# Kernel tuning notes

Measured on AMD Instinct MI355X. Metric: run time of the kernel, lower is better.

The kernel has to match this reference:

```python
import jax, jax.numpy as jnp
import numpy as np

B, S, D, H = 2, 1024, 1024, 16
HD = D // H
WINDOW = 256
FFN = 4 * D


def setup_inputs() -> dict:
    key = jax.random.key(0)
    ks = jax.random.split(key, 12)
    xav = lambda k, o, i: jax.random.normal(k, (o, i), jnp.float32) * np.sqrt(2.0 / (o + i))
    return {
        "x": jax.random.normal(ks[0], (B, S, D), jnp.float32),
        "wq": xav(ks[1], D, D), "bq": jnp.zeros((D,), jnp.float32),
        "wk": xav(ks[2], D, D), "bk": jnp.zeros((D,), jnp.float32),
        "wv": xav(ks[3], D, D), "bv": jnp.zeros((D,), jnp.float32),
        "wo": xav(ks[4], D, D), "bo": jnp.zeros((D,), jnp.float32),
        "attn_norm_w": jnp.ones((D,), jnp.float32),
        "ffn_norm_w": jnp.ones((D,), jnp.float32),
        "gate_w": xav(ks[5], FFN, D),
        "up_w": xav(ks[6], FFN, D),
        "down_w": xav(ks[7], D, FFN),
    }


def _rms(x, w):
    return x * jax.lax.rsqrt(jnp.mean(x * x, axis=-1, keepdims=True) + 1e-6) * w


def _rotate_half(x):
    x1, x2 = jnp.split(x, 2, axis=-1)
    return jnp.concatenate([-x2, x1], axis=-1)


def _rope_cos_sin(seq_len, head_dim):
    inv_freq = 1.0 / (10000.0 ** (jnp.arange(0, head_dim, 2, dtype=jnp.float32) / head_dim))
    freqs = jnp.arange(seq_len, dtype=jnp.float32)[:, None] * inv_freq[None, :]  # [S, HD/2]
    emb = jnp.concatenate([freqs, freqs], axis=-1)  # [S, HD]
    return jnp.cos(emb)[None, None], jnp.sin(emb)[None, None]  # [1,1,S,HD]


def reference(x, wq, bq, wk, bk, wv, bv, wo, bo, attn_norm_w, ffn_norm_w, gate_w, up_w, down_w):
    b, s, d = x.shape
    scale = 1.0 / np.sqrt(HD)
    residual = x
    h = _rms(x, attn_norm_w)
    q = (h @ wq.T + bq).reshape(b, s, H, HD).transpose(0, 2, 1, 3)  # [B,H,S,HD]
    k = (h @ wk.T + bk).reshape(b, s, H, HD).transpose(0, 2, 1, 3)
    v = (h @ wv.T + bv).reshape(b, s, H, HD).transpose(0, 2, 1, 3)
    cos, sin = _rope_cos_sin(s, HD)
    q = q * cos + _rotate_half(q) * sin
    k = k * cos + _rotate_half(k) * sin
    scores = jnp.einsum("bhqd,bhkd->bhqk", q, k) * scale  # dense [B,H,S,S]
    i = jnp.arange(s)[:, None]
    j = jnp.arange(s)[None, :]
    local_mask = (j <= i) & (i - j < WINDOW)  # causal sliding window
    scores = jnp.where(local_mask[None, None], scores, -jnp.inf)
    attn = jax.nn.softmax(scores, axis=-1)
    out = jnp.einsum("bhqk,bhkd->bhqd", attn, v)
    out = out.transpose(0, 2, 1, 3).reshape(b, s, d) @ wo.T + bo
    x = residual + out
    residual = x
    h = _rms(x, ffn_norm_w)
    ffn = (jax.nn.silu(h @ gate_w.T) * (h @ up_w.T)) @ down_w.T
    return (residual + ffn, attn)
```

## Files before the change

kernel.cpp:

```cpp
#include <hip/hip_runtime.h>

typedef unsigned short u16;
typedef unsigned int u32;
typedef __attribute__((ext_vector_type(8))) short short8;
typedef __attribute__((ext_vector_type(4))) float f32x4;

__device__ __forceinline__ float b2fu(u32 u) {
  union { u32 i; float f; } v; v.i = u << 16; return v.f;
}
__device__ __forceinline__ u16 f2bu(float f) {
  union { float f; u32 i; } v; v.f = f;
  u32 r = (v.i + 0x7fffu + ((v.i >> 16) & 1u)) >> 16;
  return (u16)r;
}
__device__ __forceinline__ void gl_lds16(const void* g, void* l) {
  __builtin_amdgcn_global_load_lds((const __attribute__((address_space(1))) void*)g,
                                   (__attribute__((address_space(3))) void*)l, 16, 0, 0);
}
__device__ __forceinline__ short8 ld_lds_b8(const u16* p) {
  uint2 a = *(const uint2*)p;
  uint2 b = *(const uint2*)(p + 4);
  union { u32 u[4]; short8 s; } v;
  v.u[0] = a.x; v.u[1] = a.y; v.u[2] = b.x; v.u[3] = b.y;
  return v.s;
}

__global__ __launch_bounds__(256) void cvt_weights(
    const float* __restrict__ wq, const float* __restrict__ wk,
    const float* __restrict__ wv, const float* __restrict__ wo,
    const float* __restrict__ wg, const float* __restrict__ wu,
    const float* __restrict__ wd, u16* __restrict__ dst,
    const float* __restrict__ bq, const float* __restrict__ bk,
    const float* __restrict__ bv, float* __restrict__ bqkv)
{
  if (blockIdx.x >= 16384) {
    const int s = blockIdx.x - 16384;
    const float* bsrc = (s == 0) ? bq : (s == 1) ? bk : bv;
    const int o = threadIdx.x * 4;
    *(float4*)(bqkv + s * 1024 + o) = *(const float4*)(bsrc + o);
    return;
  }
  size_t e = ((size_t)blockIdx.x * 256 + threadIdx.x) * 4;
  size_t seg = e >> 20;
  const float* src; size_t soff;
  if      (seg == 0) { src = wq; soff = e; }
  else if (seg == 1) { src = wk; soff = e - ((size_t)1 << 20); }
  else if (seg == 2) { src = wv; soff = e - ((size_t)2 << 20); }
  else if (seg == 3) { src = wo; soff = e - ((size_t)3 << 20); }
  else if (seg < 12) {
    size_t idx = e - ((size_t)4 << 20);
    int rc = (int)(idx >> 10);
    int col = (int)(idx & 1023);
    int bi = rc >> 5, j = rc & 31;
    if (j < 16) { src = wg; soff = (size_t)(bi * 16 + j) * 1024 + col; }
    else        { src = wu; soff = (size_t)(bi * 16 + j - 16) * 1024 + col; }
  }
  else { src = wd; soff = e - ((size_t)12 << 20); }
  float4 v = *(const float4*)(src + soff);
  *(ushort4*)(dst + e) = make_ushort4(f2bu(v.x), f2bu(v.y), f2bu(v.z), f2bu(v.w));
}

__global__ __launch_bounds__(256) void rmsnorm_kernel(
    const float* __restrict__ x, const float* __restrict__ w, u16* __restrict__ out)
{
  const int row = blockIdx.x;
  const int t = threadIdx.x;
  float4 v = ((const float4*)(x + (size_t)row * 1024))[t];
  float ss = v.x * v.x + v.y * v.y + v.z * v.z + v.w * v.w;
#pragma unroll
  for (int m = 32; m > 0; m >>= 1) ss += __shfl_xor(ss, m, 64);
  __shared__ float red[4];
  if ((t & 63) == 0) red[t >> 6] = ss;
  __syncthreads();
  float tot = red[0] + red[1] + red[2] + red[3];
  float r = rsqrtf(tot * (1.0f / 1024.0f) + 1e-6f);
  float4 wv = ((const float4*)w)[t];
  ushort4 o = make_ushort4(f2bu(v.x * r * wv.x), f2bu(v.y * r * wv.y),
                           f2bu(v.z * r * wv.z), f2bu(v.w * r * wv.w));
  ((ushort4*)(out + (size_t)row * 1024))[t] = o;
}

template<int TMB, int TNB, int EPI, bool HAS_BIAS, bool HAS_RES, bool SPLIT>
__global__ __launch_bounds__(256) void gemm_bt(
    const u16* __restrict__ A, const u16* __restrict__ B, float* __restrict__ C,
    const float* __restrict__ bias, const float* __restrict__ res,
    int M, int N, int K, int lda,
    u16* __restrict__ P0, u16* __restrict__ P1, u16* __restrict__ P2)
{
  constexpr int BK = 32;
  constexpr int WTM = TMB / 2, WTN = TNB / 2;
  constexpr int MT = WTM / 16, NT = WTN / 16;
  __shared__ u16 As[TMB * BK];
  __shared__ u16 Bs[TNB * BK];
  const int t = threadIdx.x;
  const int w = t >> 6, l = t & 63;
  const int wm = (w >> 1) * WTM, wn = (w & 1) * WTN;
  const int lr = l & 15, lq = l >> 4;
  const int tile_m = blockIdx.y * TMB, tile_n = blockIdx.x * TNB;
  const int kb = SPLIT ? blockIdx.z * K : 0;
  if (SPLIT) C += (size_t)blockIdx.z * M * N;

  f32x4 acc[MT][NT] = {};

  const int sr = t >> 2;
  const int scs = (((t & 3) ^ ((t >> 3) & 3)) * 8);
  const int rsw = (lq ^ ((lr >> 1) & 3)) * 8;
  const u16* Ab = A + (size_t)(tile_m + sr) * lda + kb + scs;
  const u16* Bb = B + (size_t)(tile_n + sr) * lda + kb + scs;

  for (int kk = 0; kk < K; kk += BK) {
#pragma unroll
    for (int i = 0; i < TMB / 64; ++i)
      gl_lds16(Ab + kk + (size_t)i * 64 * lda, &As[t * 8 + i * 2048]);
#pragma unroll
    for (int i = 0; i < TNB / 64; ++i)
      gl_lds16(Bb + kk + (size_t)i * 64 * lda, &Bs[t * 8 + i * 2048]);
    __syncthreads();
    short8 af[MT], bfr[NT];
#pragma unroll
    for (int mt = 0; mt < MT; ++mt)
      af[mt] = *(const short8*)&As[(wm + mt * 16 + lr) * BK + rsw];
#pragma unroll
    for (int nt = 0; nt < NT; ++nt)
      bfr[nt] = *(const short8*)&Bs[(wn + nt * 16 + lr) * BK + rsw];
#pragma unroll
    for (int mt = 0; mt < MT; ++mt)
#pragma unroll
      for (int nt = 0; nt < NT; ++nt)
        acc[mt][nt] = __builtin_amdgcn_mfma_f32_16x16x32_bf16(af[mt], bfr[nt], acc[mt][nt], 0, 0, 0);
    __syncthreads();
  }

  if (EPI == 0) {
#pragma unroll
    for (int nt = 0; nt < NT; ++nt) {
      const int col = tile_n + wn + nt * 16 + lr;
      const float bv = HAS_BIAS ? bias[col] : 0.0f;
#pragma unroll
      for (int mt = 0; mt < MT; ++mt) {
        const int row0 = tile_m + wm + mt * 16 + lq * 4;
#pragma unroll
        for (int r = 0; r < 4; ++r) {
          const size_t off = (size_t)(row0 + r) * N + col;
          float v = acc[mt][nt][r] + bv;
          if (HAS_RES) v += res[off];
          C[off] = v;
        }
      }
    }
  } else if (EPI == 1) {
    const int colbase = tile_n + wn;
    const int seg = colbase >> 10;
    const int h = (colbase >> 6) & 15;
    u16* dstb = (seg == 0) ? P0 : (seg == 1) ? P1 : P2;
    float bv[NT];
#pragma unroll
    for (int nt = 0; nt < NT; ++nt) bv[nt] = bias[colbase + nt * 16 + lr];
#pragma unroll
    for (int mt = 0; mt < MT; ++mt) {
      const int row0 = tile_m + wm + mt * 16 + lq * 4;
#pragma unroll
      for (int r = 0; r < 4; ++r) {
        const int row = row0 + r;
        const int s = row & 1023, b = row >> 10;
        u16* dst = dstb + (((size_t)(b * 16 + h) << 10) + s) * 64;
        if (seg < 2) {
#pragma unroll
          for (int np = 0; np < 2; ++np) {
            const int i = np * 16 + lr;
            const float th = (float)s * exp2f(-0.4152410118609203f * (float)i);
            float sn, cs; __sincosf(th, &sn, &cs);
            const float g0 = acc[mt][np][r] + bv[np];
            const float g2 = acc[mt][np + 2][r] + bv[np + 2];
            dst[i]      = f2bu(g0 * cs - g2 * sn);
            dst[i + 32] = f2bu(g2 * cs + g0 * sn);
          }
        } else {
#pragma unroll
          for (int nt = 0; nt < NT; ++nt)
            dst[nt * 16 + lr] = f2bu(acc[mt][nt][r] + bv[nt]);
        }
      }
    }
  } else {
#pragma unroll
    for (int nt = 0; nt < NT; nt += 2) {
      const int feat = (((tile_n + wn + nt * 16) >> 5) << 4) + lr;
#pragma unroll
      for (int mt = 0; mt < MT; ++mt) {
        const int row0 = tile_m + wm + mt * 16 + lq * 4;
#pragma unroll
        for (int r = 0; r < 4; ++r) {
          const float g = acc[mt][nt][r];
          const float u = acc[mt][nt + 1][r];
          const float a = g / (1.0f + __expf(-g)) * u;
          P0[(size_t)(row0 + r) * (N >> 1) + feat] = f2bu(a);
        }
      }
    }
  }
}

#define FPH(buf, kk, mth, dostage, dovm) do {                                                  \
    if ((mth) == 0) {                                                                          \
      _Pragma("unroll")                                                                        \
      for (int nt = 0; nt < 4; ++nt)                                                           \
        bfr[nt] = *(const short8*)&Bs[(buf) * 16384 + (wn + nt * 16 + lr) * 64 +               \
                                      (((kk) * 32 + lq * 8) ^ cxor)];                          \
    }                                                                                          \
    short8 af[4];                                                                              \
    _Pragma("unroll")                                                                          \
    for (int mt = 0; mt < 4; ++mt)                                                             \
      af[mt] = *(const short8*)&As[(buf) * 16384 + (wm + (mth) * 64 + mt * 16 + lr) * 64 +     \
                                   (((kk) * 32 + lq * 8) ^ cxor)];                             \
    if (dostage) STAGE_ALL(kt + 1);                                                            \
    __builtin_amdgcn_s_barrier();                                                              \
    asm volatile("s_waitcnt lgkmcnt(0)" ::: "memory");                                         \
    __builtin_amdgcn_sched_barrier(0);                                                         \
    __builtin_amdgcn_s_setprio(1);                                                             \
    _Pragma("unroll")                                                                          \
    for (int mt = 0; mt < 4; ++mt)                                                             \
      _Pragma("unroll")                                                                        \
      for (int nt = 0; nt < 4; ++nt)                                                           \
        acc[(mth) * 4 + mt][nt] =                                                              \
            __builtin_amdgcn_mfma_f32_16x16x32_bf16(af[mt], bfr[nt], acc[(mth) * 4 + mt][nt],  \
                                                    0, 0, 0);                                  \
    __builtin_amdgcn_s_setprio(0);                                                             \
    if (dovm) asm volatile("s_waitcnt vmcnt(0)" ::: "memory");                                 \
    __builtin_amdgcn_s_barrier();                                                              \
  } while (0)

__global__ __launch_bounds__(512, 2) void ffn1_8ph(
    const u16* __restrict__ A, const u16* __restrict__ B, u16* __restrict__ act)
{
  __shared__ u16 As[32768];
  __shared__ u16 Bs[32768];
  const int t = threadIdx.x;
  const int wid = t >> 6, l = t & 63;
  const int lr = l & 15, lq = l >> 4;
  const int wm = (wid >> 2) * 128, wn = (wid & 3) * 64;
  const int tile_m = blockIdx.y * 256, tile_n = blockIdx.x * 256;
  const int cxor = (lr & 7) * 8;

  const int srow = t >> 3;
  const int schunk = (t & 7) ^ (srow & 7);
  const u16* aRow = A + (size_t)(tile_m + srow) * 1024 + schunk * 8;
  const u16* bRow = B + (size_t)(tile_n + srow) * 1024 + schunk * 8;

  auto STAGE_ALL = [&](int kt2) {
    if (kt2 < 16) {
      const int bz2 = kt2 & 1;
      const u16* ga = aRow + kt2 * 64;
      const u16* gb = bRow + kt2 * 64;
      u16* da = As + bz2 * 16384 + t * 8;
      u16* db = Bs + bz2 * 16384 + t * 8;
      gl_lds16(ga, da);
      gl_lds16(ga + 64 * 1024, da + 4096);
      gl_lds16(ga + 128 * 1024, da + 8192);
      gl_lds16(ga + 192 * 1024, da + 12288);
      gl_lds16(gb, db);
      gl_lds16(gb + 64 * 1024, db + 4096);
      gl_lds16(gb + 128 * 1024, db + 8192);
      gl_lds16(gb + 192 * 1024, db + 12288);
    }
  };

  f32x4 acc[8][4] = {};
  short8 bfr[4];

  STAGE_ALL(0);
  asm volatile("s_waitcnt vmcnt(0)" ::: "memory");
  __builtin_amdgcn_s_barrier();

  for (int kt = 0; kt < 16; ++kt) {
    const int bz = kt & 1;
    FPH(bz, 0, 0, 1, 0);
    FPH(bz, 0, 1, 0, 0);
    FPH(bz, 1, 0, 0, 0);
    FPH(bz, 1, 1, 0, 1);
  }

#pragma unroll
  for (int nt = 0; nt < 4; nt += 2) {
    const int feat = (((tile_n + wn + nt * 16) >> 5) << 4) + lr;
#pragma unroll
    for (int mi = 0; mi < 8; ++mi) {
      const int row0 = tile_m + wm + mi * 16 + lq * 4;
#pragma unroll
      for (int r = 0; r < 4; ++r) {
        const float g = acc[mi][nt][r];
        const float u = acc[mi][nt + 1][r];
        const float a = g / (1.0f + __expf(-g)) * u;
        act[(size_t)(row0 + r) * 4096 + feat] = f2bu(a);
      }
    }
  }
}

__global__ __launch_bounds__(256) void reduce4_kernel(
    const float* __restrict__ p, const float* __restrict__ res, float* __restrict__ out)
{
  const size_t i = ((size_t)blockIdx.x * 256 + threadIdx.x) * 4;
  float4 a = *(const float4*)(p + i);
  float4 b = *(const float4*)(p + i + 2097152);
  float4 c = *(const float4*)(p + i + 2 * 2097152);
  float4 d = *(const float4*)(p + i + 3 * 2097152);
  float4 r = *(const float4*)(res + i);
  float4 o;
  o.x = r.x + a.x + b.x + c.x + d.x;
  o.y = r.y + a.y + b.y + c.y + d.y;
  o.z = r.z + a.z + b.z + c.z + d.z;
  o.w = r.w + a.w + b.w + c.w + d.w;
  *(float4*)(out + i) = o;
}

#define KP 68
#define PP 296

__global__ __launch_bounds__(256) void attn_kernel(
    const u16* __restrict__ qb, const u16* __restrict__ kb, const u16* __restrict__ vb,
    float* __restrict__ probs, u16* __restrict__ ctx)
{
  __shared__ u16 Kbuf[288 * KP];
  __shared__ u16 Vbuf[288 * KP];
  __shared__ float smax[2][32];
  __shared__ float ssum[2][32];
  u16* Pbuf = Kbuf;

  const int blk = blockIdx.x;
  const int qt = blk & 31, bh = blk >> 5;
  const int b = bh >> 4, h = bh & 15;
  const int q0 = qt << 5;
  const int kstart = (q0 >= 256) ? (q0 - 256) : 0;
  const int kend = q0 + 32;
  const int span = kend - kstart;
  const int t = threadIdx.x;
  const int w = t >> 6, l = t & 63;
  const int lr = l & 15, lq = l >> 4;
  const int mw = w & 1, nh = w >> 1;
  const size_t bhS = (size_t)bh << 10;

  {
    const u16* kg = kb + ((bhS + (size_t)kstart) << 6);
    const u16* vg = vb + ((bhS + (size_t)kstart) << 6);
    for (int idx = t; idx < 288 * 8; idx += 256) {
      const int r = idx >> 3, c = (idx & 7) << 3;
      uint4 kv4 = make_uint4(0, 0, 0, 0), vv4 = make_uint4(0, 0, 0, 0);
      if (r < span) {
        kv4 = *(const uint4*)&kg[(r << 6) + c];
        vv4 = *(const uint4*)&vg[(r << 6) + c];
      }
      *(uint2*)&Kbuf[r * KP + c]     = make_uint2(kv4.x, kv4.y);
      *(uint2*)&Kbuf[r * KP + c + 4] = make_uint2(kv4.z, kv4.w);
      *(uint2*)&Vbuf[r * KP + c]     = make_uint2(vv4.x, vv4.y);
      *(uint2*)&Vbuf[r * KP + c + 4] = make_uint2(vv4.z, vv4.w);
    }
  }
  short8 qa0, qa1;
  {
    const u16* qrow = qb + ((bhS + (size_t)(q0 + mw * 16 + lr)) << 6) + lq * 8;
    qa0 = *(const short8*)qrow;
    qa1 = *(const short8*)(qrow + 32);
  }
  __syncthreads();

  f32x4 acc[9];
#pragma unroll
  for (int i = 0; i < 9; ++i) acc[i] = (f32x4){0.f, 0.f, 0.f, 0.f};
#pragma unroll
  for (int i = 0; i < 9; ++i) {
    const int nt = nh + 2 * i;
    const u16* kr = &Kbuf[(nt * 16 + lr) * KP + lq * 8];
    short8 kf0 = ld_lds_b8(kr);
    short8 kf1 = ld_lds_b8(kr + 32);
    acc[i] = __builtin_amdgcn_mfma_f32_16x16x32_bf16(qa0, kf0, acc[i], 0, 0, 0);
    acc[i] = __builtin_amdgcn_mfma_f32_16x16x32_bf16(qa1, kf1, acc[i], 0, 0, 0);
  }

  const int rbase = mw * 16 + lq * 4;
  float rmax[4] = {-1e30f, -1e30f, -1e30f, -1e30f};
#pragma unroll
  for (int i = 0; i < 9; ++i) {
    const int jg = kstart + (nh + 2 * i) * 16 + lr;
#pragma unroll
    for (int r = 0; r < 4; ++r) {
      const int q = q0 + rbase + r;
      const bool valid = (jg >= q - 255) && (jg <= q);
      const float v = valid ? acc[i][r] * 0.125f : -1e30f;
      acc[i][r] = v;
      rmax[r] = fmaxf(rmax[r], v);
    }
  }
#pragma unroll
  for (int r = 0; r < 4; ++r) {
    float m_ = rmax[r];
    m_ = fmaxf(m_, __shfl_xor(m_, 1, 64));
    m_ = fmaxf(m_, __shfl_xor(m_, 2, 64));
    m_ = fmaxf(m_, __shfl_xor(m_, 4, 64));
    m_ = fmaxf(m_, __shfl_xor(m_, 8, 64));
    rmax[r] = m_;
  }
  if (lr == 0) {
#pragma unroll
    for (int r = 0; r < 4; ++r) smax[nh][rbase + r] = rmax[r];
  }
  __syncthreads();
#pragma unroll
  for (int r = 0; r < 4; ++r)
    rmax[r] = fmaxf(smax[0][rbase + r], smax[1][rbase + r]);
  float rsum[4] = {0.f, 0.f, 0.f, 0.f};
#pragma unroll
  for (int i = 0; i < 9; ++i)
#pragma unroll
    for (int r = 0; r < 4; ++r) {
      const float p = exp2f((acc[i][r] - rmax[r]) * 1.44269504f);
      acc[i][r] = p;
      rsum[r] += p;
    }
#pragma unroll
  for (int r = 0; r < 4; ++r) {
    float s_ = rsum[r];
    s_ += __shfl_xor(s_, 1, 64);
    s_ += __shfl_xor(s_, 2, 64);
    s_ += __shfl_xor(s_, 4, 64);
    s_ += __shfl_xor(s_, 8, 64);
    rsum[r] = s_;
  }
  if (lr == 0) {
#pragma unroll
    for (int r = 0; r < 4; ++r) ssum[nh][rbase + r] = rsum[r];
  }
  __syncthreads();

  float inv4[4];
#pragma unroll
  for (int r = 0; r < 4; ++r)
    inv4[r] = 1.0f / (ssum[0][rbase + r] + ssum[1][rbase + r]);
#pragma unroll
  for (int i = 0; i < 9; ++i) {
    const int nt = nh + 2 * i;
#pragma unroll
    for (int r = 0; r < 4; ++r)
      Pbuf[(rbase + r) * PP + nt * 16 + lr] = f2bu(acc[i][r] * inv4[r]);
  }
  __syncthreads();

  {
    const int row = t >> 3;
    const int q = q0 + row;
    const int lo = q - 255;
    const int j8 = (t & 7) << 3;
    const u16* pr0 = &Pbuf[row * PP];
    float* prow = probs + ((bhS + (size_t)q) << 10);
#pragma unroll
    for (int k = 0; k < 16; ++k) {
      const int c = j8 + (k << 6);
      float4 o0 = make_float4(0.f, 0.f, 0.f, 0.f);
      float4 o1 = make_float4(0.f, 0.f, 0.f, 0.f);
      if (c >= kstart && c < kend) {
        union { uint4 v; u16 s[8]; } pv;
        pv.v = *(const uint4*)&pr0[c - kstart];
        o0.x = (c + 0 >= lo && c + 0 <= q) ? b2fu(pv.s[0]) : 0.0f;
        o0.y = (c + 1 >= lo && c + 1 <= q) ? b2fu(pv.s[1]) : 0.0f;
        o0.z = (c + 2 >= lo && c + 2 <= q) ? b2fu(pv.s[2]) : 0.0f;
        o0.w = (c + 3 >= lo && c + 3 <= q) ? b2fu(pv.s[3]) : 0.0f;
        o1.x = (c + 4 >= lo && c + 4 <= q) ? b2fu(pv.s[4]) : 0.0f;
        o1.y = (c + 5 >= lo && c + 5 <= q) ? b2fu(pv.s[5]) : 0.0f;
        o1.z = (c + 6 >= lo && c + 6 <= q) ? b2fu(pv.s[6]) : 0.0f;
        o1.w = (c + 7 >= lo && c + 7 <= q) ? b2fu(pv.s[7]) : 0.0f;
      }
      *(float4*)&prow[c] = o0;
      *(float4*)&prow[c + 4] = o1;
    }
  }

  const int n0 = (w >> 1) * 2;
  f32x4 oacc[2] = {};
#pragma unroll
  for (int ks = 0; ks < 9; ++ks) {
    short8 pa = ld_lds_b8(&Pbuf[(mw * 16 + lr) * PP + ks * 32 + lq * 8]);
#pragma unroll
    for (int nn = 0; nn < 2; ++nn) {
      const int d = (n0 + nn) * 16 + lr;
      union { u16 u[8]; short8 s; } bf_;
#pragma unroll
      for (int jj = 0; jj < 8; ++jj)
        bf_.u[jj] = Vbuf[(ks * 32 + lq * 8 + jj) * KP + d];
      oacc[nn] = __builtin_amdgcn_mfma_f32_16x16x32_bf16(pa, bf_.s, oacc[nn], 0, 0, 0);
    }
  }
#pragma unroll
  for (int nn = 0; nn < 2; ++nn) {
    const int d = (n0 + nn) * 16 + lr;
#pragma unroll
    for (int r = 0; r < 4; ++r) {
      const int q = q0 + rbase + r;
      ctx[(((size_t)(b * 1024 + q)) << 10) + (h << 6) + d] = f2bu(oacc[nn][r]);
    }
  }
}

extern "C" void kernel_launch(void* const* d_in, const int* in_sizes, int n_in,
                              void* d_out, int out_size, void* d_ws, size_t ws_size,
                              hipStream_t stream) {
  (void)in_sizes; (void)n_in; (void)out_size; (void)ws_size;
  const float* x   = (const float*)d_in[0];
  const float* wq  = (const float*)d_in[1];
  const float* bq  = (const float*)d_in[2];
  const float* wk  = (const float*)d_in[3];
  const float* bk  = (const float*)d_in[4];
  const float* wv  = (const float*)d_in[5];
  const float* bv  = (const float*)d_in[6];
  const float* wo  = (const float*)d_in[7];
  const float* bo  = (const float*)d_in[8];
  const float* anw = (const float*)d_in[9];
  const float* fnw = (const float*)d_in[10];
  const float* wg  = (const float*)d_in[11];
  const float* wu  = (const float*)d_in[12];
  const float* wd  = (const float*)d_in[13];

  char* ws = (char*)d_ws;
  u16*   wbf  = (u16*)ws;
  float* bqkv = (float*)(ws + ((size_t)32 << 20));
  u16*   h1   = (u16*)(ws + ((size_t)32 << 20) + (16 << 10));
  char*  R    = ws + ((size_t)36 << 20) + (16 << 10);
  u16*   qbp  = (u16*)R;
  u16*   kbp  = (u16*)(R + ((size_t)4 << 20));
  u16*   vbp  = (u16*)(R + ((size_t)8 << 20));
  u16*   ctx  = (u16*)(R + ((size_t)12 << 20));
  float* x1   = (float*)(R + ((size_t)16 << 20));
  u16*   h2   = (u16*)(R + ((size_t)24 << 20));
  u16*   act  = (u16*)(R + ((size_t)28 << 20));
  float* pbuf = (float*)(R + ((size_t)44 << 20));

  float* out0  = (float*)d_out;
  float* probs = (float*)d_out + 2097152;

  cvt_weights<<<16387, 256, 0, stream>>>(wq, wk, wv, wo, wg, wu, wd, wbf,
                                          bq, bk, bv, bqkv);

  rmsnorm_kernel<<<2048, 256, 0, stream>>>(x, anw, h1);
  gemm_bt<128, 128, 1, true, false, false><<<dim3(24, 16), 256, 0, stream>>>(
      h1, wbf, nullptr, bqkv, nullptr, 2048, 3072, 1024, 1024, qbp, kbp, vbp);
  attn_kernel<<<1024, 256, 0, stream>>>(qbp, kbp, vbp, probs, ctx);
  gemm_bt<64, 128, 0, true, true, false><<<dim3(8, 32), 256, 0, stream>>>(
      ctx, wbf + ((size_t)3 << 20), x1, bo, x, 2048, 1024, 1024, 1024,
      nullptr, nullptr, nullptr);

  rmsnorm_kernel<<<2048, 256, 0, stream>>>(x1, fnw, h2);
  ffn1_8ph<<<dim3(32, 8), 512, 0, stream>>>(h2, wbf + ((size_t)4 << 20), act);
  gemm_bt<128, 128, 0, false, false, true><<<dim3(8, 16, 4), 256, 0, stream>>>(
      act, wbf + ((size_t)12 << 20), pbuf, nullptr, nullptr, 2048, 1024, 1024, 4096,
      nullptr, nullptr, nullptr);
  reduce4_kernel<<<2048, 256, 0, stream>>>(pbuf, x1, out0);
}
```

Measured before the change: 382.6 us.

## Replace down-projection GEMM with 256x256 eight-phase pipelined split-K kernel

The FFN down projection moves from the generic 128x128 gemm_bt to a dedicated 512-thread kernel with 256x256 tiles, double-buffered direct global-to-LDS loads and the same eight-phase MFMA schedule used by the FFN up/gate kernel. Larger tiles raise reuse per LDS load and are meant to cut global traffic and improve MFMA utilisation. The trade-off is only 128 blocks (4x8x4) on a 256-CU part, so under half the CUs get work. It also uses 128 KB of LDS per block despite launch_bounds(512,2), which limits occupancy.

```diff
diff --git a/kernel.cpp b/kernel.cpp
--- a/kernel.cpp
+++ b/kernel.cpp
@@ -297,6 +297,71 @@
   }
 }
 
+__global__ __launch_bounds__(512, 2) void down_8ph(
+    const u16* __restrict__ A, const u16* __restrict__ B, float* __restrict__ C)
+{
+  __shared__ u16 As[32768];
+  __shared__ u16 Bs[32768];
+  const int t = threadIdx.x;
+  const int wid = t >> 6, l = t & 63;
+  const int lr = l & 15, lq = l >> 4;
+  const int wm = (wid >> 2) * 128, wn = (wid & 3) * 64;
+  const int tile_m = blockIdx.y * 256, tile_n = blockIdx.x * 256;
+  const int kb = blockIdx.z * 1024;
+  const int cxor = (lr & 7) * 8;
+
+  const int srow = t >> 3;
+  const int schunk = (t & 7) ^ (srow & 7);
+  const u16* aRow = A + (size_t)(tile_m + srow) * 4096 + kb + schunk * 8;
+  const u16* bRow = B + (size_t)(tile_n + srow) * 4096 + kb + schunk * 8;
+
+  auto STAGE_ALL = [&](int kt2) {
+    if (kt2 < 16) {
+      const int bz2 = kt2 & 1;
+      const u16* ga = aRow + kt2 * 64;
+      const u16* gb = bRow + kt2 * 64;
+      u16* da = As + bz2 * 16384 + t * 8;
+      u16* db = Bs + bz2 * 16384 + t * 8;
+      gl_lds16(ga, da);
+      gl_lds16(ga + (size_t)64 * 4096, da + 4096);
+      gl_lds16(ga + (size_t)128 * 4096, da + 8192);
+      gl_lds16(ga + (size_t)192 * 4096, da + 12288);
+      gl_lds16(gb, db);
+      gl_lds16(gb + (size_t)64 * 4096, db + 4096);
+      gl_lds16(gb + (size_t)128 * 4096, db + 8192);
+      gl_lds16(gb + (size_t)192 * 4096, db + 12288);
+    }
+  };
+
+  f32x4 acc[8][4] = {};
+  short8 bfr[4];
+
+  STAGE_ALL(0);
+  asm volatile("s_waitcnt vmcnt(0)" ::: "memory");
+  __builtin_amdgcn_s_barrier();
+
+  for (int kt = 0; kt < 16; ++kt) {
+    const int bz = kt & 1;
+    FPH(bz, 0, 0, 1, 0);
+    FPH(bz, 0, 1, 0, 0);
+    FPH(bz, 1, 0, 0, 0);
+    FPH(bz, 1, 1, 0, 1);
+  }
+
+  float* Cp = C + (size_t)blockIdx.z * 2048 * 1024;
+#pragma unroll
+  for (int nt = 0; nt < 4; ++nt) {
+    const int col = tile_n + wn + nt * 16 + lr;
+#pragma unroll
+    for (int mi = 0; mi < 8; ++mi) {
+      const int row0 = tile_m + wm + mi * 16 + lq * 4;
+#pragma unroll
+      for (int r = 0; r < 4; ++r)
+        Cp[(size_t)(row0 + r) * 1024 + col] = acc[mi][nt][r];
+    }
+  }
+}
+
 __global__ __launch_bounds__(256) void reduce4_kernel(
     const float* __restrict__ p, const float* __restrict__ res, float* __restrict__ out)
 {
@@ -549,8 +614,6 @@
 
   rmsnorm_kernel<<<2048, 256, 0, stream>>>(x1, fnw, h2);
   ffn1_8ph<<<dim3(32, 8), 512, 0, stream>>>(h2, wbf + ((size_t)4 << 20), act);
-  gemm_bt<128, 128, 0, false, false, true><<<dim3(8, 16, 4), 256, 0, stream>>>(
-      act, wbf + ((size_t)12 << 20), pbuf, nullptr, nullptr, 2048, 1024, 1024, 4096,
-      nullptr, nullptr, nullptr);
+  down_8ph<<<dim3(4, 8, 4), 512, 0, stream>>>(act, wbf + ((size_t)12 << 20), pbuf);
   reduce4_kernel<<<2048, 256, 0, stream>>>(pbuf, x1, out0);
 }
```

Result: slower. 395.6 us (+3.4%).

## Pre-transpose V and load it into swizzled LDS via direct global-to-LDS loads

Applied to the files above, without the earlier changes.

Adds a kernel that transposes V into a [B,H,HD,S] layout. The attention kernel then loads V^T straight into LDS with global_load_lds using an XOR swizzle, so each B-operand fragment for the PV MFMA is one 16-byte LDS read instead of eight strided 2-byte reads. This costs an extra kernel launch and a round trip of V through global memory. It relies on clamping reads near the sequence end, where the probabilities are already zero.

```diff
diff --git a/kernel.cpp b/kernel.cpp
--- a/kernel.cpp
+++ b/kernel.cpp
@@ -78,6 +78,27 @@
   ushort4 o = make_ushort4(f2bu(v.x * r * wv.x), f2bu(v.y * r * wv.y),
                            f2bu(v.z * r * wv.z), f2bu(v.w * r * wv.w));
   ((ushort4*)(out + (size_t)row * 1024))[t] = o;
+}
+
+__global__ __launch_bounds__(256) void vtrans_kernel(
+    const u16* __restrict__ v, u16* __restrict__ vt)
+{
+  const int blk = blockIdx.x;
+  const int bh = blk >> 2, sq = blk & 3;
+  const int t = threadIdx.x;
+  const int sg = t >> 3, dg = t & 7;
+  const int s0 = sq * 256 + sg * 8;
+  const u16* src = v + ((size_t)bh * 1024 + s0) * 64 + dg * 8;
+  u16* dst = vt + ((size_t)bh * 64 + dg * 8) * 1024 + s0;
+  union { uint4 q; u16 s[8]; } in[8], ov;
+#pragma unroll
+  for (int i = 0; i < 8; ++i) in[i].q = *(const uint4*)(src + (size_t)i * 64);
+#pragma unroll
+  for (int j = 0; j < 8; ++j) {
+#pragma unroll
+    for (int i = 0; i < 8; ++i) ov.s[i] = in[i].s[j];
+    *(uint4*)(dst + (size_t)j * 1024) = ov.q;
+  }
 }
 
 template<int TMB, int TNB, int EPI, bool HAS_BIAS, bool HAS_RES, bool SPLIT>
@@ -318,11 +339,11 @@
 #define PP 296
 
 __global__ __launch_bounds__(256) void attn_kernel(
-    const u16* __restrict__ qb, const u16* __restrict__ kb, const u16* __restrict__ vb,
+    const u16* __restrict__ qb, const u16* __restrict__ kb, const u16* __restrict__ vtb,
     float* __restrict__ probs, u16* __restrict__ ctx)
 {
   __shared__ u16 Kbuf[288 * KP];
-  __shared__ u16 Vbuf[288 * KP];
+  __shared__ u16 VT[64 * 320];
   __shared__ float smax[2][32];
   __shared__ float ssum[2][32];
   u16* Pbuf = Kbuf;
@@ -342,18 +363,21 @@
 
   {
     const u16* kg = kb + ((bhS + (size_t)kstart) << 6);
-    const u16* vg = vb + ((bhS + (size_t)kstart) << 6);
     for (int idx = t; idx < 288 * 8; idx += 256) {
       const int r = idx >> 3, c = (idx & 7) << 3;
-      uint4 kv4 = make_uint4(0, 0, 0, 0), vv4 = make_uint4(0, 0, 0, 0);
-      if (r < span) {
-        kv4 = *(const uint4*)&kg[(r << 6) + c];
-        vv4 = *(const uint4*)&vg[(r << 6) + c];
-      }
+      uint4 kv4 = make_uint4(0, 0, 0, 0);
+      if (r < span) kv4 = *(const uint4*)&kg[(r << 6) + c];
       *(uint2*)&Kbuf[r * KP + c]     = make_uint2(kv4.x, kv4.y);
       *(uint2*)&Kbuf[r * KP + c + 4] = make_uint2(kv4.z, kv4.w);
-      *(uint2*)&Vbuf[r * KP + c]     = make_uint2(vv4.x, vv4.y);
-      *(uint2*)&Vbuf[r * KP + c + 4] = make_uint2(vv4.z, vv4.w);
+    }
+    const u16* vg = vtb + ((size_t)bh << 16) + kstart;
+#pragma unroll
+    for (int i = 0; i < 10; ++i) {
+      const int cd = t + i * 256;
+      const int d = cd / 40, sr2 = cd - d * 40;
+      int csrc = (sr2 & ~7) | ((sr2 & 7) ^ (d & 7));
+      if (csrc >= 36) csrc = 35;
+      gl_lds16(vg + (size_t)d * 1024 + csrc * 8, &VT[cd * 8]);
     }
   }
   short8 qa0, qa1;
@@ -479,14 +503,13 @@
 #pragma unroll
   for (int ks = 0; ks < 9; ++ks) {
     short8 pa = ld_lds_b8(&Pbuf[(mw * 16 + lr) * PP + ks * 32 + lq * 8]);
+    const int ci = ks * 4 + lq;
 #pragma unroll
     for (int nn = 0; nn < 2; ++nn) {
       const int d = (n0 + nn) * 16 + lr;
-      union { u16 u[8]; short8 s; } bf_;
-#pragma unroll
-      for (int jj = 0; jj < 8; ++jj)
-        bf_.u[jj] = Vbuf[(ks * 32 + lq * 8 + jj) * KP + d];
-      oacc[nn] = __builtin_amdgcn_mfma_f32_16x16x32_bf16(pa, bf_.s, oacc[nn], 0, 0, 0);
+      const int slot = (ci & ~7) | ((ci & 7) ^ (d & 7));
+      short8 bf = *(const short8*)&VT[d * 320 + slot * 8];
+      oacc[nn] = __builtin_amdgcn_mfma_f32_16x16x32_bf16(pa, bf, oacc[nn], 0, 0, 0);
     }
   }
 #pragma unroll
@@ -532,6 +555,7 @@
   u16*   h2   = (u16*)(R + ((size_t)24 << 20));
   u16*   act  = (u16*)(R + ((size_t)28 << 20));
   float* pbuf = (float*)(R + ((size_t)44 << 20));
+  u16*   vtb  = (u16*)(R + ((size_t)76 << 20));
 
   float* out0  = (float*)d_out;
   float* probs = (float*)d_out + 2097152;
@@ -542,7 +566,8 @@
   rmsnorm_kernel<<<2048, 256, 0, stream>>>(x, anw, h1);
   gemm_bt<128, 128, 1, true, false, false><<<dim3(24, 16), 256, 0, stream>>>(
       h1, wbf, nullptr, bqkv, nullptr, 2048, 3072, 1024, 1024, qbp, kbp, vbp);
-  attn_kernel<<<1024, 256, 0, stream>>>(qbp, kbp, vbp, probs, ctx);
+  vtrans_kernel<<<128, 256, 0, stream>>>(vbp, vtb);
+  attn_kernel<<<1024, 256, 0, stream>>>(qbp, kbp, vtb, probs, ctx);
   gemm_bt<64, 128, 0, true, true, false><<<dim3(8, 32), 256, 0, stream>>>(
       ctx, wbf + ((size_t)3 << 20), x1, bo, x, 2048, 1024, 1024, 1024,
       nullptr, nullptr, nullptr);
```

Measured after the change: 384.5 us. About the same (+0.5%).
